# Kernel tuning notes

Hardware: AMD Instinct MI355X
Metric: run time of the kernel (lower is better)

## Reference

```python
import jax, jax.numpy as jnp
import numpy as np

N_NODES = 50000


def gcn_conv(x, W, b, src, dst, n_nodes):
    """PyG GCNConv: add self-loops, symmetric deg normalization, x@W then aggregate."""
    h = x @ W  # [N, out]
    # add self loops
    loop = jnp.arange(n_nodes, dtype=src.dtype)
    s = jnp.concatenate([src, loop])
    d = jnp.concatenate([dst, loop])
    # degree at target nodes (includes self loop)
    deg = jax.ops.segment_sum(jnp.ones_like(d, dtype=h.dtype), d, num_segments=n_nodes)
    dinv = jnp.where(deg > 0, jax.lax.rsqrt(deg), 0.0)
    norm = dinv[s] * dinv[d]  # [E+N]
    msgs = h[s] * norm[:, None]  # [E+N, out]
    out = jax.ops.segment_sum(msgs, d, num_segments=n_nodes)
    return out + b


def setup_inputs() -> dict:
    key = jax.random.key(0)
    k = jax.random.split(key, 8)
    d_in, d_h, d_z = 128, 128, 32
    x = jax.random.normal(k[0], (N_NODES, d_in), dtype=jnp.float32)
    edge_index = jax.random.randint(k[1], (2, 600000), 0, N_NODES, dtype=jnp.int64)
    y_edge_index = jax.random.randint(k[2], (2, 200000), 0, N_NODES, dtype=jnp.int64)
    W1 = jax.random.normal(k[3], (d_in, d_h), dtype=jnp.float32) / np.sqrt(d_in)
    b1 = jnp.zeros((d_h,), dtype=jnp.float32)
    W_mu = jax.random.normal(k[4], (d_h, d_z), dtype=jnp.float32) / np.sqrt(d_h)
    b_mu = jnp.zeros((d_z,), dtype=jnp.float32)
    W_ls = jax.random.normal(k[5], (d_h, d_z), dtype=jnp.float32) / np.sqrt(d_h)
    b_ls = jnp.zeros((d_z,), dtype=jnp.float32)
    return {"x": x, "edge_index": edge_index, "y_edge_index": y_edge_index,
            "W1": W1, "b1": b1, "W_mu": W_mu, "b_mu": b_mu, "W_ls": W_ls, "b_ls": b_ls}


def reference(x, edge_index, y_edge_index, W1, b1, W_mu, b_mu, W_ls, b_ls):
    ei = jnp.concatenate([edge_index, y_edge_index], axis=1)
    src, dst = ei[0], ei[1]
    n = x.shape[0]
    h = jax.nn.relu(gcn_conv(x, W1, b1, src, dst, n))
    z_mu = gcn_conv(h, W_mu, b_mu, src, dst, n)
    z_logstd = gcn_conv(h, W_ls, b_ls, src, dst, n)
    return (z_mu, z_logstd)
```

## Files before the change

### kernel.cpp

```cpp
#include <hip/hip_runtime.h>
#include <hip/hip_bf16.h>

#define CAP 64
#define NODES_PER_BLOCK 4

typedef __attribute__((ext_vector_type(8))) short short8;
typedef __attribute__((ext_vector_type(4))) float f32x4;

__device__ __forceinline__ unsigned short f2bf(float f) {
    unsigned int u = __float_as_uint(f);
    unsigned int r = (u + 0x7fffu + ((u >> 16) & 1u)) >> 16;
    return (unsigned short)r;
}
__device__ __forceinline__ float bf_lo(unsigned int u) { return __uint_as_float(u << 16); }
__device__ __forceinline__ float bf_hi(unsigned int u) { return __uint_as_float(u & 0xffff0000u); }

__global__ void prep_wt_kernel(const float* __restrict__ W1, const float* __restrict__ Wmu,
                               const float* __restrict__ Wls,
                               unsigned short* __restrict__ W1T, unsigned short* __restrict__ W2T) {
    int idx = blockIdx.x * 256 + threadIdx.x;
    if (idx < 128 * 128) {
        int c = idx >> 7, k = idx & 127;
        W1T[c * 128 + k] = f2bf(W1[k * 128 + c]);
    } else {
        int i2 = idx - 128 * 128;
        if (i2 < 64 * 128) {
            int c = i2 >> 7, k = i2 & 127;
            float v = (c < 32) ? Wmu[k * 32 + c] : Wls[k * 32 + (c - 32)];
            W2T[c * 128 + k] = f2bf(v);
        }
    }
}

__global__ __launch_bounds__(256) void fused_fill_gemm1(
    const int* __restrict__ e1, const int* __restrict__ e2,
    const float* __restrict__ x, const unsigned short* __restrict__ W1T,
    int* __restrict__ counts, unsigned short* __restrict__ edges,
    unsigned short* __restrict__ h1, int E1, int E2, int M, int nbe) {
    int bid = blockIdx.x;
    if (bid < nbe) {
        int e = bid * 256 + threadIdx.x;
        int s, d;
        if (e < E1) {
            s = e1[e]; d = e1[E1 + e];
        } else if (e < E1 + E2) {
            int t = e - E1;
            s = e2[t]; d = e2[E2 + t];
        } else return;
        int pos = atomicAdd(&counts[d], 1);
        if (pos < CAP) edges[d * CAP + pos] = (unsigned short)s;
        return;
    }
    int wv = ((bid - nbe) << 2) | (threadIdx.x >> 6);
    int brow = wv << 4;
    if (brow >= M) return;
    int lane = threadIdx.x & 63;
    int r = lane & 15, g = lane >> 4;
    const float* ar = x + (size_t)(brow + r) * 128;
    f32x4 acc[8] = {};
#pragma unroll
    for (int kk = 0; kk < 4; ++kk) {
        float4 a0 = *(const float4*)(ar + kk * 32 + g * 8);
        float4 a1 = *(const float4*)(ar + kk * 32 + g * 8 + 4);
        short8 af;
        af[0] = (short)f2bf(a0.x); af[1] = (short)f2bf(a0.y);
        af[2] = (short)f2bf(a0.z); af[3] = (short)f2bf(a0.w);
        af[4] = (short)f2bf(a1.x); af[5] = (short)f2bf(a1.y);
        af[6] = (short)f2bf(a1.z); af[7] = (short)f2bf(a1.w);
#pragma unroll
        for (int ct = 0; ct < 8; ++ct) {
            short8 b = *(const short8*)(W1T + (size_t)(ct * 16 + r) * 128 + kk * 32 + g * 8);
            acc[ct] = __builtin_amdgcn_mfma_f32_16x16x32_bf16(af, b, acc[ct], 0, 0, 0);
        }
    }
#pragma unroll
    for (int ct = 0; ct < 8; ++ct) {
#pragma unroll
        for (int rr = 0; rr < 4; ++rr) {
            int row = brow + 4 * g + rr;
            h1[(size_t)row * 128 + ct * 16 + r] = f2bf(acc[ct][rr]);
        }
    }
}

__global__ void agg_h_kernel(const unsigned short* __restrict__ h1,
                             const unsigned short* __restrict__ edges,
                             const int* __restrict__ counts, const float* __restrict__ b1,
                             unsigned short* __restrict__ h, int n) {
    int wave = threadIdx.x >> 6, lane = threadIdx.x & 63;
    int v = blockIdx.x * NODES_PER_BLOCK + wave;
    if (v >= n) return;
    int cv = counts[v];
    int cnt = min(cv, CAP);
    const unsigned short* el = edges + (size_t)v * CAP;
    float ax = 0.f, ay = 0.f;
#pragma unroll 4
    for (int e = 0; e < cnt; ++e) {
        int s = el[e];
        float w = rsqrtf((float)(counts[s] + 1));
        unsigned int u = ((const unsigned int*)(h1 + (size_t)s * 128))[lane];
        ax = fmaf(w, bf_lo(u), ax);
        ay = fmaf(w, bf_hi(u), ay);
    }
    float di = rsqrtf((float)(cv + 1));
    unsigned int su = ((const unsigned int*)(h1 + (size_t)v * 128))[lane];
    float ox = di * fmaf(di, bf_lo(su), ax) + b1[2 * lane];
    float oy = di * fmaf(di, bf_hi(su), ay) + b1[2 * lane + 1];
    unsigned int pack = (unsigned int)f2bf(fmaxf(ox, 0.f)) |
                        ((unsigned int)f2bf(fmaxf(oy, 0.f)) << 16);
    ((unsigned int*)(h + (size_t)v * 128))[lane] = pack;
}

__global__ __launch_bounds__(256) void gemm2_kernel(const unsigned short* __restrict__ h,
                                                    const unsigned short* __restrict__ W2T,
                                                    const int* __restrict__ counts,
                                                    unsigned short* __restrict__ g2, int M) {
    int wv = (blockIdx.x << 2) | (threadIdx.x >> 6);
    int brow = wv << 4;
    if (brow >= M) return;
    int lane = threadIdx.x & 63;
    int r = lane & 15, g = lane >> 4;
    const unsigned short* ar = h + (size_t)(brow + r) * 128;
    f32x4 acc[4] = {};
#pragma unroll
    for (int kk = 0; kk < 4; ++kk) {
        short8 af = *(const short8*)(ar + kk * 32 + g * 8);
#pragma unroll
        for (int ct = 0; ct < 4; ++ct) {
            short8 b = *(const short8*)(W2T + (size_t)(ct * 16 + r) * 128 + kk * 32 + g * 8);
            acc[ct] = __builtin_amdgcn_mfma_f32_16x16x32_bf16(af, b, acc[ct], 0, 0, 0);
        }
    }
#pragma unroll
    for (int ct = 0; ct < 4; ++ct) {
#pragma unroll
        for (int rr = 0; rr < 4; ++rr) {
            int row = brow + 4 * g + rr;
            float sc = rsqrtf((float)(counts[row] + 1));
            g2[(size_t)row * 64 + ct * 16 + r] = f2bf(sc * acc[ct][rr]);
        }
    }
}

__global__ void agg_out_kernel(const unsigned short* __restrict__ g,
                               const unsigned short* __restrict__ edges,
                               const int* __restrict__ counts,
                               const float* __restrict__ bmu, const float* __restrict__ bls,
                               float* __restrict__ out, int n) {
    int wave = threadIdx.x >> 6, lane = threadIdx.x & 63;
    int v = blockIdx.x * NODES_PER_BLOCK + wave;
    if (v >= n) return;
    int cv = counts[v];
    int cnt = min(cv, CAP);
    const unsigned short* el = edges + (size_t)v * CAP;
    float acc = 0.f;
#pragma unroll 4
    for (int e = 0; e < cnt; ++e) {
        int s = el[e];
        acc += __uint_as_float((unsigned int)g[(size_t)s * 64 + lane] << 16);
    }
    acc += __uint_as_float((unsigned int)g[(size_t)v * 64 + lane] << 16);
    float res = rsqrtf((float)(cv + 1)) * acc;
    if (lane < 32) {
        out[(size_t)v * 32 + lane] = res + bmu[lane];
    } else {
        out[(size_t)n * 32 + (size_t)v * 32 + (lane - 32)] = res + bls[lane - 32];
    }
}

extern "C" void kernel_launch(void* const* d_in, const int* in_sizes, int n_in,
                              void* d_out, int out_size, void* d_ws, size_t ws_size,
                              hipStream_t stream) {
    const float* x   = (const float*)d_in[0];
    const int*   ei  = (const int*)d_in[1];
    const int*   yei = (const int*)d_in[2];
    const float* W1  = (const float*)d_in[3];
    const float* b1  = (const float*)d_in[4];
    const float* Wmu = (const float*)d_in[5];
    const float* bmu = (const float*)d_in[6];
    const float* Wls = (const float*)d_in[7];
    const float* bls = (const float*)d_in[8];

    const int N  = in_sizes[0] / 128;
    const int E1 = in_sizes[1] / 2;
    const int E2 = in_sizes[2] / 2;
    const int E  = E1 + E2;

    size_t off = 0;
    auto alloc = [&](size_t bytes) {
        char* p = (char*)d_ws + off;
        off += (bytes + 255) & ~(size_t)255;
        return (void*)p;
    };
    int*            counts = (int*)alloc((size_t)N * 4);
    unsigned short* edges  = (unsigned short*)alloc((size_t)N * CAP * 2);
    unsigned short* h1     = (unsigned short*)alloc((size_t)N * 128 * 2);
    unsigned short* h      = (unsigned short*)alloc((size_t)N * 128 * 2);
    unsigned short* g2     = (unsigned short*)alloc((size_t)N * 64 * 2);
    unsigned short* W1T    = (unsigned short*)alloc(128 * 128 * 2);
    unsigned short* W2T    = (unsigned short*)alloc(64 * 128 * 2);
    (void)ws_size; (void)n_in; (void)out_size;

    const int NB_E = (E + 255) / 256;
    const int NB_G1 = (N / 16 + 3) / 4;
    const int NB_AG = (N + NODES_PER_BLOCK - 1) / NODES_PER_BLOCK;

    hipMemsetAsync(counts, 0, (size_t)N * 4, stream);
    prep_wt_kernel<<<(128 * 128 + 64 * 128 + 255) / 256, 256, 0, stream>>>(W1, Wmu, Wls, W1T, W2T);

    fused_fill_gemm1<<<NB_E + NB_G1, 256, 0, stream>>>(ei, yei, x, W1T, counts, edges, h1,
                                                       E1, E2, N, NB_E);

    agg_h_kernel<<<NB_AG, 64 * NODES_PER_BLOCK, 0, stream>>>(h1, edges, counts, b1, h, N);

    gemm2_kernel<<<NB_G1, 256, 0, stream>>>(h, W2T, counts, g2, N);

    agg_out_kernel<<<NB_AG, 64 * NODES_PER_BLOCK, 0, stream>>>(g2, edges, counts, bmu, bls,
                                                               (float*)d_out, N);
}
```

Baseline: 254.3 us.

## Partition edge fill by XCD, precompute dinv and pre-scale GEMM1 output

Splits the fused fill+GEMM1 kernel. Edge filling now runs as 8 interleaved block groups, each inserting only destinations in its node range, so atomics on a node's counter come from one XCD. Because GEMM1 now needs degrees, it runs after the fill and a new dinv kernel precomputes rsqrt degrees. GEMM1 output is pre-scaled by the source dinv, which removes the per-edge counts[s] gather and rsqrt from the first aggregation. In exchange every edge index is read 8 times, fill and GEMM1 no longer overlap, and two extra launches are added.

```diff
diff --git a/kernel.cpp b/kernel.cpp
--- a/kernel.cpp
+++ b/kernel.cpp
@@ -32,26 +32,39 @@
     }
 }
 
-__global__ __launch_bounds__(256) void fused_fill_gemm1(
+__global__ __launch_bounds__(256) void fill_xcd_kernel(
     const int* __restrict__ e1, const int* __restrict__ e2,
-    const float* __restrict__ x, const unsigned short* __restrict__ W1T,
     int* __restrict__ counts, unsigned short* __restrict__ edges,
-    unsigned short* __restrict__ h1, int E1, int E2, int M, int nbe) {
-    int bid = blockIdx.x;
-    if (bid < nbe) {
-        int e = bid * 256 + threadIdx.x;
+    int E1, int E2, int rng) {
+    int g  = blockIdx.x & 7;
+    int lo = g * rng, hi = lo + rng;
+    int base = (blockIdx.x >> 3) * 2048;
+#pragma unroll
+    for (int i = 0; i < 8; ++i) {
+        int e = base + i * 256 + threadIdx.x;
         int s, d;
         if (e < E1) {
             s = e1[e]; d = e1[E1 + e];
         } else if (e < E1 + E2) {
             int t = e - E1;
             s = e2[t]; d = e2[E2 + t];
-        } else return;
-        int pos = atomicAdd(&counts[d], 1);
-        if (pos < CAP) edges[d * CAP + pos] = (unsigned short)s;
-        return;
-    }
-    int wv = ((bid - nbe) << 2) | (threadIdx.x >> 6);
+        } else continue;
+        if (d >= lo && d < hi) {
+            int pos = atomicAdd(&counts[d], 1);
+            if (pos < CAP) edges[d * CAP + pos] = (unsigned short)s;
+        }
+    }
+}
+
+__global__ void dinv_kernel(const int* __restrict__ counts, float* __restrict__ dinv, int n) {
+    int i = blockIdx.x * blockDim.x + threadIdx.x;
+    if (i < n) dinv[i] = rsqrtf((float)(counts[i] + 1));
+}
+
+__global__ __launch_bounds__(256) void gemm1_kernel(
+    const float* __restrict__ x, const unsigned short* __restrict__ W1T,
+    const float* __restrict__ dinv, unsigned short* __restrict__ h1, int M) {
+    int wv = (blockIdx.x << 2) | (threadIdx.x >> 6);
     int brow = wv << 4;
     if (brow >= M) return;
     int lane = threadIdx.x & 63;
@@ -78,34 +91,34 @@
 #pragma unroll
         for (int rr = 0; rr < 4; ++rr) {
             int row = brow + 4 * g + rr;
-            h1[(size_t)row * 128 + ct * 16 + r] = f2bf(acc[ct][rr]);
+            h1[(size_t)row * 128 + ct * 16 + r] = f2bf(dinv[row] * acc[ct][rr]);
         }
     }
 }
 
 __global__ void agg_h_kernel(const unsigned short* __restrict__ h1,
                              const unsigned short* __restrict__ edges,
-                             const int* __restrict__ counts, const float* __restrict__ b1,
-                             unsigned short* __restrict__ h, int n) {
+                             const int* __restrict__ counts, const float* __restrict__ dinv,
+                             const float* __restrict__ b1, unsigned short* __restrict__ h, int n) {
     int wave = threadIdx.x >> 6, lane = threadIdx.x & 63;
     int v = blockIdx.x * NODES_PER_BLOCK + wave;
     if (v >= n) return;
-    int cv = counts[v];
-    int cnt = min(cv, CAP);
+    int cnt = min(counts[v], CAP);
     const unsigned short* el = edges + (size_t)v * CAP;
     float ax = 0.f, ay = 0.f;
 #pragma unroll 4
     for (int e = 0; e < cnt; ++e) {
         int s = el[e];
-        float w = rsqrtf((float)(counts[s] + 1));
         unsigned int u = ((const unsigned int*)(h1 + (size_t)s * 128))[lane];
-        ax = fmaf(w, bf_lo(u), ax);
-        ay = fmaf(w, bf_hi(u), ay);
-    }
-    float di = rsqrtf((float)(cv + 1));
+        ax += bf_lo(u);
+        ay += bf_hi(u);
+    }
     unsigned int su = ((const unsigned int*)(h1 + (size_t)v * 128))[lane];
-    float ox = di * fmaf(di, bf_lo(su), ax) + b1[2 * lane];
-    float oy = di * fmaf(di, bf_hi(su), ay) + b1[2 * lane + 1];
+    ax += bf_lo(su);
+    ay += bf_hi(su);
+    float di = dinv[v];
+    float ox = di * ax + b1[2 * lane];
+    float oy = di * ay + b1[2 * lane + 1];
     unsigned int pack = (unsigned int)f2bf(fmaxf(ox, 0.f)) |
                         ((unsigned int)f2bf(fmaxf(oy, 0.f)) << 16);
     ((unsigned int*)(h + (size_t)v * 128))[lane] = pack;
@@ -113,7 +126,7 @@
 
 __global__ __launch_bounds__(256) void gemm2_kernel(const unsigned short* __restrict__ h,
                                                     const unsigned short* __restrict__ W2T,
-                                                    const int* __restrict__ counts,
+                                                    const float* __restrict__ dinv,
                                                     unsigned short* __restrict__ g2, int M) {
     int wv = (blockIdx.x << 2) | (threadIdx.x >> 6);
     int brow = wv << 4;
@@ -136,22 +149,20 @@
 #pragma unroll
         for (int rr = 0; rr < 4; ++rr) {
             int row = brow + 4 * g + rr;
-            float sc = rsqrtf((float)(counts[row] + 1));
-            g2[(size_t)row * 64 + ct * 16 + r] = f2bf(sc * acc[ct][rr]);
+            g2[(size_t)row * 64 + ct * 16 + r] = f2bf(dinv[row] * acc[ct][rr]);
         }
     }
 }
 
 __global__ void agg_out_kernel(const unsigned short* __restrict__ g,
                                const unsigned short* __restrict__ edges,
-                               const int* __restrict__ counts,
+                               const int* __restrict__ counts, const float* __restrict__ dinv,
                                const float* __restrict__ bmu, const float* __restrict__ bls,
                                float* __restrict__ out, int n) {
     int wave = threadIdx.x >> 6, lane = threadIdx.x & 63;
     int v = blockIdx.x * NODES_PER_BLOCK + wave;
     if (v >= n) return;
-    int cv = counts[v];
-    int cnt = min(cv, CAP);
+    int cnt = min(counts[v], CAP);
     const unsigned short* el = edges + (size_t)v * CAP;
     float acc = 0.f;
 #pragma unroll 4
@@ -160,7 +171,7 @@
         acc += __uint_as_float((unsigned int)g[(size_t)s * 64 + lane] << 16);
     }
     acc += __uint_as_float((unsigned int)g[(size_t)v * 64 + lane] << 16);
-    float res = rsqrtf((float)(cv + 1)) * acc;
+    float res = dinv[v] * acc;
     if (lane < 32) {
         out[(size_t)v * 32 + lane] = res + bmu[lane];
     } else {
@@ -193,6 +204,7 @@
         return (void*)p;
     };
     int*            counts = (int*)alloc((size_t)N * 4);
+    float*          dinv   = (float*)alloc((size_t)N * 4);
     unsigned short* edges  = (unsigned short*)alloc((size_t)N * CAP * 2);
     unsigned short* h1     = (unsigned short*)alloc((size_t)N * 128 * 2);
     unsigned short* h      = (unsigned short*)alloc((size_t)N * 128 * 2);
@@ -201,20 +213,22 @@
     unsigned short* W2T    = (unsigned short*)alloc(64 * 128 * 2);
     (void)ws_size; (void)n_in; (void)out_size;
 
-    const int NB_E = (E + 255) / 256;
-    const int NB_G1 = (N / 16 + 3) / 4;
+    const int NB_N  = (N + 255) / 256;
+    const int NB_C  = (E + 2047) / 2048;
+    const int NB_G  = (N / 16 + 3) / 4;
     const int NB_AG = (N + NODES_PER_BLOCK - 1) / NODES_PER_BLOCK;
+    const int rng   = (N + 7) / 8;
 
     hipMemsetAsync(counts, 0, (size_t)N * 4, stream);
     prep_wt_kernel<<<(128 * 128 + 64 * 128 + 255) / 256, 256, 0, stream>>>(W1, Wmu, Wls, W1T, W2T);
 
-    fused_fill_gemm1<<<NB_E + NB_G1, 256, 0, stream>>>(ei, yei, x, W1T, counts, edges, h1,
-                                                       E1, E2, N, NB_E);
-
-    agg_h_kernel<<<NB_AG, 64 * NODES_PER_BLOCK, 0, stream>>>(h1, edges, counts, b1, h, N);
-
-    gemm2_kernel<<<NB_G1, 256, 0, stream>>>(h, W2T, counts, g2, N);
-
-    agg_out_kernel<<<NB_AG, 64 * NODES_PER_BLOCK, 0, stream>>>(g2, edges, counts, bmu, bls,
+    fill_xcd_kernel<<<8 * NB_C, 256, 0, stream>>>(ei, yei, counts, edges, E1, E2, rng);
+    dinv_kernel<<<NB_N, 256, 0, stream>>>(counts, dinv, N);
+
+    gemm1_kernel<<<NB_G, 256, 0, stream>>>(x, W1T, dinv, h1, N);
+    agg_h_kernel<<<NB_AG, 64 * NODES_PER_BLOCK, 0, stream>>>(h1, edges, counts, dinv, b1, h, N);
+
+    gemm2_kernel<<<NB_G, 256, 0, stream>>>(h, W2T, dinv, g2, N);
+    agg_out_kernel<<<NB_AG, 64 * NODES_PER_BLOCK, 0, stream>>>(g2, edges, counts, dinv, bmu, bls,
                                                                (float*)d_out, N);
 }
```

New measurement: 232.1 us. 8.7% less time.

## Fuse layer-1 aggregation with GEMM2 and partition edge fill by destination range

Applied to the files above, without the earlier changes.

Merges weight prep into the edge-fill kernel. The fill is split into 8 destination-range groups, so each block only does atomics for destinations in its slice, which is meant to improve atomic locality. GEMM1 is now a separate kernel that runs after the fill and pre-scales its rows by the source degree, so the layer-1 aggregation no longer looks up counts[s] per edge. Aggregation of h then feeds a per-node LDS dot product with W2T, removing the h round trip through global memory and one launch. In exchange, the edge index arrays are read 8 times, GEMM1 can no longer overlap with the fill, and GEMM2 moves from MFMA to scalar FMAs.

```diff
diff --git a/kernel.cpp b/kernel.cpp
--- a/kernel.cpp
+++ b/kernel.cpp
@@ -14,44 +14,54 @@
 }
 __device__ __forceinline__ float bf_lo(unsigned int u) { return __uint_as_float(u << 16); }
 __device__ __forceinline__ float bf_hi(unsigned int u) { return __uint_as_float(u & 0xffff0000u); }
-
-__global__ void prep_wt_kernel(const float* __restrict__ W1, const float* __restrict__ Wmu,
-                               const float* __restrict__ Wls,
-                               unsigned short* __restrict__ W1T, unsigned short* __restrict__ W2T) {
-    int idx = blockIdx.x * 256 + threadIdx.x;
-    if (idx < 128 * 128) {
-        int c = idx >> 7, k = idx & 127;
-        W1T[c * 128 + k] = f2bf(W1[k * 128 + c]);
-    } else {
-        int i2 = idx - 128 * 128;
-        if (i2 < 64 * 128) {
-            int c = i2 >> 7, k = i2 & 127;
-            float v = (c < 32) ? Wmu[k * 32 + c] : Wls[k * 32 + (c - 32)];
-            W2T[c * 128 + k] = f2bf(v);
-        }
-    }
-}
-
-__global__ __launch_bounds__(256) void fused_fill_gemm1(
+__device__ __forceinline__ float bfu(unsigned short u) { return __uint_as_float((unsigned int)u << 16); }
+
+__global__ __launch_bounds__(256) void prep_fill_kernel(
+    const float* __restrict__ W1, const float* __restrict__ Wmu, const float* __restrict__ Wls,
+    unsigned short* __restrict__ W1T, unsigned short* __restrict__ W2T,
     const int* __restrict__ e1, const int* __restrict__ e2,
-    const float* __restrict__ x, const unsigned short* __restrict__ W1T,
     int* __restrict__ counts, unsigned short* __restrict__ edges,
-    unsigned short* __restrict__ h1, int E1, int E2, int M, int nbe) {
+    int E1, int E2, int rng, int nbp) {
     int bid = blockIdx.x;
-    if (bid < nbe) {
-        int e = bid * 256 + threadIdx.x;
+    if (bid < nbp) {
+        int idx = bid * 256 + threadIdx.x;
+        if (idx < 128 * 128) {
+            int c = idx >> 7, k = idx & 127;
+            W1T[c * 128 + k] = f2bf(W1[k * 128 + c]);
+        } else {
+            int i2 = idx - 128 * 128;
+            if (i2 < 64 * 128) {
+                int c = i2 >> 7, k = i2 & 127;
+                float v = (c < 32) ? Wmu[k * 32 + c] : Wls[k * 32 + (c - 32)];
+                W2T[c * 128 + k] = f2bf(v);
+            }
+        }
+        return;
+    }
+    int g  = bid & 7;
+    int lo = g * rng, hi = lo + rng;
+    int base = ((bid - nbp) >> 3) * 2048;
+#pragma unroll
+    for (int i = 0; i < 8; ++i) {
+        int e = base + i * 256 + threadIdx.x;
         int s, d;
         if (e < E1) {
             s = e1[e]; d = e1[E1 + e];
         } else if (e < E1 + E2) {
             int t = e - E1;
             s = e2[t]; d = e2[E2 + t];
-        } else return;
-        int pos = atomicAdd(&counts[d], 1);
-        if (pos < CAP) edges[d * CAP + pos] = (unsigned short)s;
-        return;
-    }
-    int wv = ((bid - nbe) << 2) | (threadIdx.x >> 6);
+        } else continue;
+        if (d >= lo && d < hi) {
+            int pos = atomicAdd(&counts[d], 1);
+            if (pos < CAP) edges[d * CAP + pos] = (unsigned short)s;
+        }
+    }
+}
+
+__global__ __launch_bounds__(256) void gemm1_kernel(
+    const float* __restrict__ x, const unsigned short* __restrict__ W1T,
+    const int* __restrict__ counts, unsigned short* __restrict__ h1, int M) {
+    int wv = (blockIdx.x << 2) | (threadIdx.x >> 6);
     int brow = wv << 4;
     if (brow >= M) return;
     int lane = threadIdx.x & 63;
@@ -78,67 +88,52 @@
 #pragma unroll
         for (int rr = 0; rr < 4; ++rr) {
             int row = brow + 4 * g + rr;
-            h1[(size_t)row * 128 + ct * 16 + r] = f2bf(acc[ct][rr]);
-        }
-    }
-}
-
-__global__ void agg_h_kernel(const unsigned short* __restrict__ h1,
-                             const unsigned short* __restrict__ edges,
-                             const int* __restrict__ counts, const float* __restrict__ b1,
-                             unsigned short* __restrict__ h, int n) {
+            float sc = rsqrtf((float)(counts[row] + 1));
+            h1[(size_t)row * 128 + ct * 16 + r] = f2bf(sc * acc[ct][rr]);
+        }
+    }
+}
+
+__global__ __launch_bounds__(256) void agg_h_g2_kernel(
+    const unsigned short* __restrict__ h1, const unsigned short* __restrict__ edges,
+    const int* __restrict__ counts, const float* __restrict__ b1,
+    const unsigned short* __restrict__ W2T, unsigned short* __restrict__ g2, int n) {
+    __shared__ float h_lds[NODES_PER_BLOCK][128];
     int wave = threadIdx.x >> 6, lane = threadIdx.x & 63;
     int v = blockIdx.x * NODES_PER_BLOCK + wave;
-    if (v >= n) return;
-    int cv = counts[v];
-    int cnt = min(cv, CAP);
-    const unsigned short* el = edges + (size_t)v * CAP;
-    float ax = 0.f, ay = 0.f;
-#pragma unroll 4
-    for (int e = 0; e < cnt; ++e) {
-        int s = el[e];
-        float w = rsqrtf((float)(counts[s] + 1));
-        unsigned int u = ((const unsigned int*)(h1 + (size_t)s * 128))[lane];
-        ax = fmaf(w, bf_lo(u), ax);
-        ay = fmaf(w, bf_hi(u), ay);
-    }
-    float di = rsqrtf((float)(cv + 1));
-    unsigned int su = ((const unsigned int*)(h1 + (size_t)v * 128))[lane];
-    float ox = di * fmaf(di, bf_lo(su), ax) + b1[2 * lane];
-    float oy = di * fmaf(di, bf_hi(su), ay) + b1[2 * lane + 1];
-    unsigned int pack = (unsigned int)f2bf(fmaxf(ox, 0.f)) |
-                        ((unsigned int)f2bf(fmaxf(oy, 0.f)) << 16);
-    ((unsigned int*)(h + (size_t)v * 128))[lane] = pack;
-}
-
-__global__ __launch_bounds__(256) void gemm2_kernel(const unsigned short* __restrict__ h,
-                                                    const unsigned short* __restrict__ W2T,
-                                                    const int* __restrict__ counts,
-                                                    unsigned short* __restrict__ g2, int M) {
-    int wv = (blockIdx.x << 2) | (threadIdx.x >> 6);
-    int brow = wv << 4;
-    if (brow >= M) return;
-    int lane = threadIdx.x & 63;
-    int r = lane & 15, g = lane >> 4;
-    const unsigned short* ar = h + (size_t)(brow + r) * 128;
-    f32x4 acc[4] = {};
-#pragma unroll
-    for (int kk = 0; kk < 4; ++kk) {
-        short8 af = *(const short8*)(ar + kk * 32 + g * 8);
-#pragma unroll
-        for (int ct = 0; ct < 4; ++ct) {
-            short8 b = *(const short8*)(W2T + (size_t)(ct * 16 + r) * 128 + kk * 32 + g * 8);
-            acc[ct] = __builtin_amdgcn_mfma_f32_16x16x32_bf16(af, b, acc[ct], 0, 0, 0);
-        }
-    }
-#pragma unroll
-    for (int ct = 0; ct < 4; ++ct) {
-#pragma unroll
-        for (int rr = 0; rr < 4; ++rr) {
-            int row = brow + 4 * g + rr;
-            float sc = rsqrtf((float)(counts[row] + 1));
-            g2[(size_t)row * 64 + ct * 16 + r] = f2bf(sc * acc[ct][rr]);
-        }
+    bool active = v < n;
+    float di = 0.f;
+    if (active) {
+        int cv = counts[v];
+        int cnt = min(cv, CAP);
+        di = rsqrtf((float)(cv + 1));
+        const unsigned short* el = edges + (size_t)v * CAP;
+        float ax = 0.f, ay = 0.f;
+#pragma unroll 8
+        for (int e = 0; e < cnt; ++e) {
+            int s = el[e];
+            unsigned int u = ((const unsigned int*)(h1 + (size_t)s * 128))[lane];
+            ax += bf_lo(u);
+            ay += bf_hi(u);
+        }
+        unsigned int su = ((const unsigned int*)(h1 + (size_t)v * 128))[lane];
+        ax += bf_lo(su);
+        ay += bf_hi(su);
+        h_lds[wave][2 * lane]     = fmaxf(di * ax + b1[2 * lane], 0.f);
+        h_lds[wave][2 * lane + 1] = fmaxf(di * ay + b1[2 * lane + 1], 0.f);
+    }
+    __syncthreads();
+    if (active) {
+        const unsigned short* wrow = W2T + (size_t)lane * 128;
+        float acc = 0.f;
+#pragma unroll
+        for (int kk = 0; kk < 16; ++kk) {
+            short8 wv8 = *(const short8*)(wrow + kk * 8);
+#pragma unroll
+            for (int j = 0; j < 8; ++j)
+                acc = fmaf(h_lds[wave][kk * 8 + j], bfu((unsigned short)wv8[j]), acc);
+        }
+        g2[(size_t)v * 64 + lane] = f2bf(di * acc);
     }
 }
 
@@ -154,12 +149,12 @@
     int cnt = min(cv, CAP);
     const unsigned short* el = edges + (size_t)v * CAP;
     float acc = 0.f;
-#pragma unroll 4
+#pragma unroll 8
     for (int e = 0; e < cnt; ++e) {
         int s = el[e];
-        acc += __uint_as_float((unsigned int)g[(size_t)s * 64 + lane] << 16);
-    }
-    acc += __uint_as_float((unsigned int)g[(size_t)v * 64 + lane] << 16);
+        acc += bfu(g[(size_t)s * 64 + lane]);
+    }
+    acc += bfu(g[(size_t)v * 64 + lane]);
     float res = rsqrtf((float)(cv + 1)) * acc;
     if (lane < 32) {
         out[(size_t)v * 32 + lane] = res + bmu[lane];
@@ -195,25 +190,26 @@
     int*            counts = (int*)alloc((size_t)N * 4);
     unsigned short* edges  = (unsigned short*)alloc((size_t)N * CAP * 2);
     unsigned short* h1     = (unsigned short*)alloc((size_t)N * 128 * 2);
-    unsigned short* h      = (unsigned short*)alloc((size_t)N * 128 * 2);
     unsigned short* g2     = (unsigned short*)alloc((size_t)N * 64 * 2);
     unsigned short* W1T    = (unsigned short*)alloc(128 * 128 * 2);
     unsigned short* W2T    = (unsigned short*)alloc(64 * 128 * 2);
     (void)ws_size; (void)n_in; (void)out_size;
 
-    const int NB_E = (E + 255) / 256;
-    const int NB_G1 = (N / 16 + 3) / 4;
+    const int NB_P  = (128 * 128 + 64 * 128) / 256;
+    const int NB_C  = (E + 2047) / 2048;
+    const int NB_G  = (N / 16 + 3) / 4;
     const int NB_AG = (N + NODES_PER_BLOCK - 1) / NODES_PER_BLOCK;
+    const int rng   = (N + 7) / 8;
 
     hipMemsetAsync(counts, 0, (size_t)N * 4, stream);
-    prep_wt_kernel<<<(128 * 128 + 64 * 128 + 255) / 256, 256, 0, stream>>>(W1, Wmu, Wls, W1T, W2T);
-
-    fused_fill_gemm1<<<NB_E + NB_G1, 256, 0, stream>>>(ei, yei, x, W1T, counts, edges, h1,
-                                                       E1, E2, N, NB_E);
-
-    agg_h_kernel<<<NB_AG, 64 * NODES_PER_BLOCK, 0, stream>>>(h1, edges, counts, b1, h, N);
-
-    gemm2_kernel<<<NB_G1, 256, 0, stream>>>(h, W2T, counts, g2, N);
+
+    prep_fill_kernel<<<NB_P + 8 * NB_C, 256, 0, stream>>>(W1, Wmu, Wls, W1T, W2T,
+                                                          ei, yei, counts, edges, E1, E2,
+                                                          rng, NB_P);
+
+    gemm1_kernel<<<NB_G, 256, 0, stream>>>(x, W1T, counts, h1, N);
+
+    agg_h_g2_kernel<<<NB_AG, 64 * NODES_PER_BLOCK, 0, stream>>>(h1, edges, counts, b1, W2T, g2, N);
 
     agg_out_kernel<<<NB_AG, 64 * NODES_PER_BLOCK, 0, stream>>>(g2, edges, counts, bmu, bls,
                                                                (float*)d_out, N);
```

After: 295.2 us. +16.1%, slower.
